# Kernel tuning notes

Measured on AMD Instinct MI355X. Metric: run time of the kernel, lower is better.

The kernel has to match this reference:

```python
import jax, jax.numpy as jnp
import numpy as np

B, N, F = 4, 3000, 128

def setup_inputs() -> dict:
    key = jax.random.key(0)
    k1, k2, k3, k4 = jax.random.split(key, 4)
    x = jax.random.normal(k1, (B, N, F), dtype=jnp.float32)
    adj = jax.random.uniform(k2, (B, N, N), dtype=jnp.float32)
    h0 = jax.random.normal(k3, (B, N, F), dtype=jnp.float32)
    stdv = 1.0 / np.sqrt(F)
    theta = jax.random.uniform(k4, (F, F), dtype=jnp.float32, minval=-stdv, maxval=stdv)
    return {
        "x": x, "adj": adj, "h0": h0, "theta": theta,
        "lamda": jnp.float32(0.5), "alpha": jnp.float32(0.1), "l": 4,
    }

def _normalize_adj(adj):
    # add self loops, then D^{-1/2} A D^{-1/2} via elementwise row/col scaling
    # (same math as diag-embed + inverse + two bmms in the original)
    n = adj.shape[1]
    adj = adj + jnp.eye(n, dtype=adj.dtype)
    deg = jnp.sum(adj, axis=2)                      # [B, N]
    d_inv_sqrt = jax.lax.rsqrt(deg)                 # [B, N]
    return d_inv_sqrt[:, :, None] * adj * d_inv_sqrt[:, None, :]

def reference(x, adj, h0, theta, lamda, alpha, l):
    adj_n = _normalize_adj(adj)
    beta = jnp.log(lamda / l + 1.0)
    hi = jnp.einsum('bnm,bmf->bnf', adj_n, x)       # aggregation
    support = (1.0 - alpha) * hi + alpha * h0       # variant=False path
    r = support
    out = beta * jnp.einsum('bnf,fg->bng', support, theta) + (1.0 - beta) * r
    return out
```

## Files before the change

### kernel.cpp

```cpp
#include <hip/hip_runtime.h>
#include <hip/hip_bf16.h>
#include <math.h>

#define BB 4
#define NN 3000
#define FF 128
#define NKC 94
#define NIT 188

typedef __bf16 bf16x8 __attribute__((ext_vector_type(8)));
typedef __bf16 bf16x4 __attribute__((ext_vector_type(4)));
typedef float  f32x4  __attribute__((ext_vector_type(4)));

__global__ __launch_bounds__(256) void k_deg(const float* __restrict__ adj,
                                             float* __restrict__ dis) {
    int wid  = (blockIdx.x * 256 + threadIdx.x) >> 6;
    int lane = threadIdx.x & 63;
    if (wid >= BB * NN) return;
    const float4* row = (const float4*)(adj + (size_t)wid * NN);
    float s = 0.f;
    for (int c = lane; c < NN / 4; c += 64) {
        float4 v = row[c];
        s += (v.x + v.y) + (v.z + v.w);
    }
    for (int off = 32; off > 0; off >>= 1) s += __shfl_down(s, off, 64);
    if (lane == 0) dis[wid] = 1.0f / sqrtf(s + 1.0f);
}

__global__ __launch_bounds__(256) void k_xpk(const float* __restrict__ x,
                                             const float* __restrict__ dis,
                                             __bf16* __restrict__ xpk) {
    int b  = blockIdx.y, kc = blockIdx.x;
    int t  = threadIdx.x, w = t >> 6, l = t & 63;
    int m  = l & 15, q = l >> 4;
    #pragma unroll
    for (int h = 0; h < 2; ++h) {
        int nt = w + h * 4;
        int f  = nt * 16 + m;
        bf16x8 v;
        #pragma unroll
        for (int j = 0; j < 8; ++j) {
            int k = kc * 32 + q * 8 + j;
            float val = 0.f;
            if (k < NN) val = dis[b * NN + k] * x[((size_t)b * NN + k) * FF + f];
            v[j] = (__bf16)val;
        }
        *(bf16x8*)(xpk + ((size_t)(b * 8 + nt) * NKC + kc) * 512 + l * 8) = v;
    }
}

__global__ __launch_bounds__(256) void k_agg(const float* __restrict__ adj,
                                             const __bf16* __restrict__ xpk,
                                             const float* __restrict__ x,
                                             const float* __restrict__ h0,
                                             const float* __restrict__ dis,
                                             float* __restrict__ support,
                                             const float* __restrict__ alpha_p) {
    __shared__ __bf16 tile[16][264];
    const int b  = blockIdx.y;
    const int it = blockIdx.x;
    const int i0 = it * 16;
    const int t  = threadIdx.x, w = t >> 6, l = t & 63;
    const int m  = l & 15, quad = l >> 4;
    const __bf16* B0 = xpk + ((size_t)(b * 8 + 2 * w) * NKC) * 512 + l * 8;
    const __bf16* B1 = B0 + (size_t)NKC * 512;
    f32x4 acc0 = {0.f, 0.f, 0.f, 0.f};
    f32x4 acc1 = {0.f, 0.f, 0.f, 0.f};
    for (int c = 0; c < 12; ++c) {
        int k0 = c * 256;
        #pragma unroll
        for (int i = 0; i < 4; ++i) {
            int row = i * 4 + w;
            int col = k0 + l * 4;
            float4 v = {0.f, 0.f, 0.f, 0.f};
            if (i0 + row < NN && col < NN)
                v = *(const float4*)(adj + ((size_t)b * NN + i0 + row) * NN + col);
            __bf16* tp = &tile[row][l * 4];
            tp[0] = (__bf16)v.x; tp[1] = (__bf16)v.y;
            tp[2] = (__bf16)v.z; tp[3] = (__bf16)v.w;
        }
        __syncthreads();
        int nk = (c == 11) ? 6 : 8;
        #pragma unroll 2
        for (int kcl = 0; kcl < nk; ++kcl) {
            int kc = c * 8 + kcl;
            bf16x8 a  = *(const bf16x8*)&tile[m][kcl * 32 + quad * 8];
            bf16x8 b0 = *(const bf16x8*)(B0 + (size_t)kc * 512);
            bf16x8 b1 = *(const bf16x8*)(B1 + (size_t)kc * 512);
            acc0 = __builtin_amdgcn_mfma_f32_16x16x32_bf16(a, b0, acc0, 0, 0, 0);
            acc1 = __builtin_amdgcn_mfma_f32_16x16x32_bf16(a, b1, acc1, 0, 0, 0);
        }
        __syncthreads();
    }
    const float alpha = *alpha_p;
    const int n0 = w * 32;
    #pragma unroll
    for (int r = 0; r < 4; ++r) {
        int irow = i0 + quad * 4 + r;
        if (irow < NN) {
            float  di   = dis[b * NN + irow];
            size_t base = ((size_t)b * NN + irow) * FF;
            int c0 = n0 + m;
            float hi0 = di * acc0[r] + di * di * x[base + c0];
            support[base + c0] = (1.f - alpha) * hi0 + alpha * h0[base + c0];
            int c1 = n0 + 16 + m;
            float hi1 = di * acc1[r] + di * di * x[base + c1];
            support[base + c1] = (1.f - alpha) * hi1 + alpha * h0[base + c1];
        }
    }
}

__global__ __launch_bounds__(256) void k_out(const float* __restrict__ support,
                                             const float* __restrict__ theta,
                                             float* __restrict__ out,
                                             const float* __restrict__ lamda_p,
                                             const int* __restrict__ l_p) {
    __shared__ __bf16 th[FF * FF];
    __shared__ float  srow[16 * FF];
    int b  = blockIdx.y;
    int r0 = blockIdx.x * 16;
    for (int idx = threadIdx.x; idx < FF * FF; idx += 256) th[idx] = (__bf16)theta[idx];
    for (int idx = threadIdx.x; idx < 16 * FF; idx += 256) {
        int r = idx >> 7;
        int irow = r0 + r;
        srow[idx] = (irow < NN) ? support[((size_t)b * NN + irow) * FF + (idx & 127)] : 0.f;
    }
    __syncthreads();
    float beta = logf(*lamda_p / (float)(*l_p) + 1.0f);
    float omb  = 1.0f - beta;
    int c0 = (threadIdx.x & 31) * 4;
    int rp = (threadIdx.x >> 5) * 2;
    float a0[4] = {0.f, 0.f, 0.f, 0.f};
    float a1[4] = {0.f, 0.f, 0.f, 0.f};
    for (int g = 0; g < FF; ++g) {
        float s0 = srow[rp * FF + g];
        float s1 = srow[rp * FF + FF + g];
        bf16x4 t4 = *(const bf16x4*)&th[g * FF + c0];
        #pragma unroll
        for (int cc = 0; cc < 4; ++cc) {
            float tv = (float)t4[cc];
            a0[cc] += s0 * tv;
            a1[cc] += s1 * tv;
        }
    }
    int irow0 = r0 + rp;
    if (irow0 < NN) {
        float4 o;
        o.x = beta * a0[0] + omb * srow[rp * FF + c0 + 0];
        o.y = beta * a0[1] + omb * srow[rp * FF + c0 + 1];
        o.z = beta * a0[2] + omb * srow[rp * FF + c0 + 2];
        o.w = beta * a0[3] + omb * srow[rp * FF + c0 + 3];
        *(float4*)&out[((size_t)b * NN + irow0) * FF + c0] = o;
    }
    int irow1 = irow0 + 1;
    if (irow1 < NN) {
        float4 o;
        o.x = beta * a1[0] + omb * srow[(rp + 1) * FF + c0 + 0];
        o.y = beta * a1[1] + omb * srow[(rp + 1) * FF + c0 + 1];
        o.z = beta * a1[2] + omb * srow[(rp + 1) * FF + c0 + 2];
        o.w = beta * a1[3] + omb * srow[(rp + 1) * FF + c0 + 3];
        *(float4*)&out[((size_t)b * NN + irow1) * FF + c0] = o;
    }
}

extern "C" void kernel_launch(void* const* d_in, const int* in_sizes, int n_in,
                              void* d_out, int out_size, void* d_ws, size_t ws_size,
                              hipStream_t stream) {
    const float* x      = (const float*)d_in[0];
    const float* adj    = (const float*)d_in[1];
    const float* h0     = (const float*)d_in[2];
    const float* theta  = (const float*)d_in[3];
    const float* lamda  = (const float*)d_in[4];
    const float* alpha  = (const float*)d_in[5];
    const int*   l      = (const int*)d_in[6];
    float* out = (float*)d_out;

    char*   ws      = (char*)d_ws;
    float*  dis     = (float*)ws;
    __bf16* xpk     = (__bf16*)(ws + 65536);
    float*  support = (float*)(ws + 4 * 1024 * 1024);

    k_deg<<<dim3((BB * NN) / 4), 256, 0, stream>>>(adj, dis);
    k_xpk<<<dim3(NKC, BB), 256, 0, stream>>>(x, dis, xpk);
    k_agg<<<dim3(NIT, BB), 256, 0, stream>>>(adj, xpk, x, h0, dis, support, alpha);
    k_out<<<dim3(NIT, BB), 256, 0, stream>>>(support, theta, out, lamda, l);
}
```

Measured before the change: 300.6 us.

## Fuse theta projection into aggregation kernel using MFMA on pre-packed theta

Removes the separate k_out kernel and the support buffer round-trip to global memory. The aggregation kernel now writes the support tile to shared memory as bf16 and multiplies it by a pre-packed bf16 theta using MFMA, then writes the final output directly. A small k_thpk kernel packs theta into MFMA B-operand layout. This cuts global traffic and the scalar FMA loop of k_out, at the cost of rounding support to bf16 before the theta matmul.

Result: faster. 287.0 us (-4.5%).

```diff
diff --git a/kernel.cpp b/kernel.cpp
--- a/kernel.cpp
+++ b/kernel.cpp
@@ -49,19 +49,40 @@
     }
 }
 
+__global__ __launch_bounds__(256) void k_thpk(const float* __restrict__ theta,
+                                              __bf16* __restrict__ thpk) {
+    int kc = blockIdx.x;
+    int t  = threadIdx.x, w = t >> 6, l = t & 63;
+    int m  = l & 15, q = l >> 4;
+    #pragma unroll
+    for (int h = 0; h < 2; ++h) {
+        int nt = w + h * 4;
+        bf16x8 v;
+        #pragma unroll
+        for (int j = 0; j < 8; ++j) {
+            int k = kc * 32 + q * 8 + j;
+            v[j] = (__bf16)theta[k * FF + nt * 16 + m];
+        }
+        *(bf16x8*)(thpk + ((size_t)(nt * 4 + kc)) * 512 + l * 8) = v;
+    }
+}
+
 __global__ __launch_bounds__(256) void k_agg(const float* __restrict__ adj,
                                              const __bf16* __restrict__ xpk,
+                                             const __bf16* __restrict__ thpk,
                                              const float* __restrict__ x,
                                              const float* __restrict__ h0,
                                              const float* __restrict__ dis,
-                                             float* __restrict__ support,
-                                             const float* __restrict__ alpha_p) {
+                                             float* __restrict__ out,
+                                             const float* __restrict__ alpha_p,
+                                             const float* __restrict__ lamda_p,
+                                             const int* __restrict__ l_p) {
     __shared__ __bf16 tile[16][264];
     const int b  = blockIdx.y;
-    const int it = blockIdx.x;
-    const int i0 = it * 16;
+    const int i0 = blockIdx.x * 16;
     const int t  = threadIdx.x, w = t >> 6, l = t & 63;
     const int m  = l & 15, quad = l >> 4;
+    const int n0 = w * 32;
     const __bf16* B0 = xpk + ((size_t)(b * 8 + 2 * w) * NKC) * 512 + l * 8;
     const __bf16* B1 = B0 + (size_t)NKC * 512;
     f32x4 acc0 = {0.f, 0.f, 0.f, 0.f};
@@ -93,73 +114,46 @@
         __syncthreads();
     }
     const float alpha = *alpha_p;
-    const int n0 = w * 32;
+    const float beta  = logf(*lamda_p / (float)(*l_p) + 1.0f);
+    float s0v[4], s1v[4];
+    #pragma unroll
+    for (int r = 0; r < 4; ++r) {
+        int row  = quad * 4 + r;
+        int irow = i0 + row;
+        float s0 = 0.f, s1 = 0.f;
+        if (irow < NN) {
+            float  di   = dis[b * NN + irow];
+            size_t base = ((size_t)b * NN + irow) * FF;
+            int c0 = n0 + m, c1 = n0 + 16 + m;
+            s0 = (1.f - alpha) * (di * acc0[r] + di * di * x[base + c0]) + alpha * h0[base + c0];
+            s1 = (1.f - alpha) * (di * acc1[r] + di * di * x[base + c1]) + alpha * h0[base + c1];
+        }
+        s0v[r] = s0; s1v[r] = s1;
+        tile[row][n0 + m]      = (__bf16)s0;
+        tile[row][n0 + 16 + m] = (__bf16)s1;
+    }
+    __syncthreads();
+    f32x4 o0 = {0.f, 0.f, 0.f, 0.f};
+    f32x4 o1 = {0.f, 0.f, 0.f, 0.f};
+    const __bf16* T0 = thpk + (size_t)(2 * w * 4) * 512 + l * 8;
+    const __bf16* T1 = T0 + 4 * 512;
+    #pragma unroll
+    for (int kc = 0; kc < 4; ++kc) {
+        bf16x8 a   = *(const bf16x8*)&tile[m][kc * 32 + quad * 8];
+        bf16x8 tb0 = *(const bf16x8*)(T0 + (size_t)kc * 512);
+        bf16x8 tb1 = *(const bf16x8*)(T1 + (size_t)kc * 512);
+        o0 = __builtin_amdgcn_mfma_f32_16x16x32_bf16(a, tb0, o0, 0, 0, 0);
+        o1 = __builtin_amdgcn_mfma_f32_16x16x32_bf16(a, tb1, o1, 0, 0, 0);
+    }
+    const float omb = 1.f - beta;
     #pragma unroll
     for (int r = 0; r < 4; ++r) {
         int irow = i0 + quad * 4 + r;
         if (irow < NN) {
-            float  di   = dis[b * NN + irow];
             size_t base = ((size_t)b * NN + irow) * FF;
-            int c0 = n0 + m;
-            float hi0 = di * acc0[r] + di * di * x[base + c0];
-            support[base + c0] = (1.f - alpha) * hi0 + alpha * h0[base + c0];
-            int c1 = n0 + 16 + m;
-            float hi1 = di * acc1[r] + di * di * x[base + c1];
-            support[base + c1] = (1.f - alpha) * hi1 + alpha * h0[base + c1];
+            out[base + n0 + m]      = beta * o0[r] + omb * s0v[r];
+            out[base + n0 + 16 + m] = beta * o1[r] + omb * s1v[r];
         }
-    }
-}
-
-__global__ __launch_bounds__(256) void k_out(const float* __restrict__ support,
-                                             const float* __restrict__ theta,
-                                             float* __restrict__ out,
-                                             const float* __restrict__ lamda_p,
-                                             const int* __restrict__ l_p) {
-    __shared__ __bf16 th[FF * FF];
-    __shared__ float  srow[16 * FF];
-    int b  = blockIdx.y;
-    int r0 = blockIdx.x * 16;
-    for (int idx = threadIdx.x; idx < FF * FF; idx += 256) th[idx] = (__bf16)theta[idx];
-    for (int idx = threadIdx.x; idx < 16 * FF; idx += 256) {
-        int r = idx >> 7;
-        int irow = r0 + r;
-        srow[idx] = (irow < NN) ? support[((size_t)b * NN + irow) * FF + (idx & 127)] : 0.f;
-    }
-    __syncthreads();
-    float beta = logf(*lamda_p / (float)(*l_p) + 1.0f);
-    float omb  = 1.0f - beta;
-    int c0 = (threadIdx.x & 31) * 4;
-    int rp = (threadIdx.x >> 5) * 2;
-    float a0[4] = {0.f, 0.f, 0.f, 0.f};
-    float a1[4] = {0.f, 0.f, 0.f, 0.f};
-    for (int g = 0; g < FF; ++g) {
-        float s0 = srow[rp * FF + g];
-        float s1 = srow[rp * FF + FF + g];
-        bf16x4 t4 = *(const bf16x4*)&th[g * FF + c0];
-        #pragma unroll
-        for (int cc = 0; cc < 4; ++cc) {
-            float tv = (float)t4[cc];
-            a0[cc] += s0 * tv;
-            a1[cc] += s1 * tv;
-        }
-    }
-    int irow0 = r0 + rp;
-    if (irow0 < NN) {
-        float4 o;
-        o.x = beta * a0[0] + omb * srow[rp * FF + c0 + 0];
-        o.y = beta * a0[1] + omb * srow[rp * FF + c0 + 1];
-        o.z = beta * a0[2] + omb * srow[rp * FF + c0 + 2];
-        o.w = beta * a0[3] + omb * srow[rp * FF + c0 + 3];
-        *(float4*)&out[((size_t)b * NN + irow0) * FF + c0] = o;
-    }
-    int irow1 = irow0 + 1;
-    if (irow1 < NN) {
-        float4 o;
-        o.x = beta * a1[0] + omb * srow[(rp + 1) * FF + c0 + 0];
-        o.y = beta * a1[1] + omb * srow[(rp + 1) * FF + c0 + 1];
-        o.z = beta * a1[2] + omb * srow[(rp + 1) * FF + c0 + 2];
-        o.w = beta * a1[3] + omb * srow[(rp + 1) * FF + c0 + 3];
-        *(float4*)&out[((size_t)b * NN + irow1) * FF + c0] = o;
     }
 }
 
@@ -175,13 +169,14 @@
     const int*   l      = (const int*)d_in[6];
     float* out = (float*)d_out;
 
-    char*   ws      = (char*)d_ws;
-    float*  dis     = (float*)ws;
-    __bf16* xpk     = (__bf16*)(ws + 65536);
-    float*  support = (float*)(ws + 4 * 1024 * 1024);
+    char*   ws   = (char*)d_ws;
+    float*  dis  = (float*)ws;
+    __bf16* xpk  = (__bf16*)(ws + 65536);
+    __bf16* thpk = (__bf16*)(ws + 3200000);
 
     k_deg<<<dim3((BB * NN) / 4), 256, 0, stream>>>(adj, dis);
     k_xpk<<<dim3(NKC, BB), 256, 0, stream>>>(x, dis, xpk);
-    k_agg<<<dim3(NIT, BB), 256, 0, stream>>>(adj, xpk, x, h0, dis, support, alpha);
-    k_out<<<dim3(NIT, BB), 256, 0, stream>>>(support, theta, out, lamda, l);
+    k_thpk<<<dim3(4), 256, 0, stream>>>(theta, thpk);
+    k_agg<<<dim3(NIT, BB), 256, 0, stream>>>(adj, xpk, thpk, x, h0, dis, out,
+                                             alpha, lamda, l);
 }
```
